# Optimization experiments

Measured on AMD Instinct MI355X. Metric: run time of the kernel, lower is better.

The kernel has to match this reference:

```python
import jax, jax.numpy as jnp
import numpy as np

B, LQ, LK, D, DV = 8, 2048, 2048, 128, 128


def setup_inputs() -> dict:
    key = jax.random.key(0)
    ks = jax.random.split(key, 6)
    return {
        "query": jax.random.normal(ks[0], (B, LQ, D), dtype=jnp.float32),
        "key": jax.random.normal(ks[1], (B, LK, D), dtype=jnp.float32),
        "value": jax.random.normal(ks[2], (B, LK, DV), dtype=jnp.float32),
        "Wq": jax.random.normal(ks[3], (D, D), dtype=jnp.float32) * 0.08,
        "Wk": jax.random.normal(ks[4], (D, D), dtype=jnp.float32) * 0.08,
        "Wv": jax.random.normal(ks[5], (DV, DV), dtype=jnp.float32) * 0.08,
        "attention_mask": jnp.ones((B, 1, LK), dtype=jnp.int32),
    }


def reference(query, key, value, Wq, Wk, Wv, attention_mask):
    # Linear projections (right-multiplication, as in `x @ W`)
    q = query @ Wq          # [B, lq, n_ed]
    k = key @ Wk            # [B, lk, n_ed]
    v = value @ Wv          # [B, lk, n_ev]
    scale = 1.0 / np.sqrt(q.shape[-1])
    scores = jnp.einsum("bqd,bkd->bqk", q, k) * scale  # [B, lq, lk]
    # additive mask: 0 where attend, -inf where mask==0 (broadcasts)
    mask_vals = jnp.where(attention_mask == 0, -jnp.inf, 0.0).astype(scores.dtype)
    scores = scores + mask_vals
    attn = jax.nn.softmax(scores, axis=-1)
    return attn @ v         # [B, lq, n_ev]
```

## Files before the change

### kernel.cpp

```cpp
#include <hip/hip_runtime.h>
#include <hip/hip_bf16.h>

typedef unsigned short u16;
typedef unsigned int u32;
typedef __attribute__((ext_vector_type(8))) short s8v;
typedef __attribute__((ext_vector_type(4))) float f4v;
typedef __attribute__((ext_vector_type(16))) float f16v;

#define B_N 8
#define L_Q 2048
#define L_K 2048
#define DIM 128
#define KT  64
#define KSPLIT 4
#define KCHUNK (L_K / KSPLIT)
#define NIT (KCHUNK / KT)

__device__ __forceinline__ u16 f2bf(float f) {
  union { float f; unsigned u; } v; v.f = f;
  return (u16)((v.u + 0x7fffu + ((v.u >> 16) & 1u)) >> 16);
}
__device__ __forceinline__ float bf2f(u16 u) {
  union { u32 u; float f; } v; v.u = ((u32)u) << 16; return v.f;
}
__device__ __forceinline__ u32 packbf2(float a, float b) {
  union { __hip_bfloat162 h; u32 u; } v;
  v.h = __float22bfloat162_rn(make_float2(a, b));
  return v.u;
}
__device__ __forceinline__ void async16(const u16* g, u16* l) {
  __builtin_amdgcn_global_load_lds(
      (const __attribute__((address_space(1))) u32*)(const void*)g,
      (__attribute__((address_space(3))) u32*)(void*)l, 16, 0, 0);
}


__global__ __launch_bounds__(256) void wprep(
    const float* __restrict__ Wq, const float* __restrict__ Wk,
    const float* __restrict__ Wv, u16* __restrict__ wbuf) {
  const int which = blockIdx.x;
  const int tid = threadIdx.x;
  const float* W = (which == 0) ? Wq : (which == 1) ? Wk : Wv;
  const float wscale = (which == 0) ? (1.44269504089f / 11.3137084990f) : 1.0f;
  u16* dst = wbuf + which * 16384;
#pragma unroll
  for (int i = 0; i < 16; ++i) {
    int f4i = tid + i * 256;
    float4 w4 = *(const float4*)(W + f4i * 4);
    int k = f4i >> 5, col = (f4i & 31) * 4;
    int ks = k >> 5, qd = (k & 31) >> 3, j = k & 7;
    float wv4[4] = {w4.x, w4.y, w4.z, w4.w};
#pragma unroll
    for (int c = 0; c < 4; ++c) {
      int n = col + c;
      dst[(ks * 8 + (n >> 4)) * 512 + (qd * 16 + (n & 15)) * 8 + j] = f2bf(wv4[c] * wscale);
    }
  }
}

__global__ __launch_bounds__(256, 3) void proj_mfma(
    const float* __restrict__ query, const float* __restrict__ key,
    const float* __restrict__ value, const u16* __restrict__ wbuf,
    u16* __restrict__ qp, u16* __restrict__ kp, u16* __restrict__ vp) {
  __shared__ __align__(16) u16 Wf[16384];
  __shared__ __align__(16) u16 Fb[8192];
  const int tid = threadIdx.x;
  const int bi = blockIdx.x;
  const int which = bi >> 8;
  const int sub = bi & 255;
  const int b = sub >> 5;
  const int rt = sub & 31;
  const float* X = (which == 0) ? query : (which == 1) ? key : value;
  const u16* Wfg = wbuf + which * 16384;

  const int w = tid >> 6, lane = tid & 63;
  const int ln = lane & 15, quad = lane >> 4;

#pragma unroll
  for (int c = 0; c < 8; ++c) {
    int cg = w * 8 + c;
    async16(Wfg + (size_t)(cg * 64 + lane) * 8, Wf + cg * 512);
  }

  const int xrow = rt * 64 + w * 16 + ln;
  const float* Xr = X + ((size_t)b * L_Q + xrow) * DIM;

  s8v a[4];
#pragma unroll
  for (int ks = 0; ks < 4; ++ks) {
    float4 xa = *(const float4*)(Xr + ks * 32 + quad * 8);
    float4 xb = *(const float4*)(Xr + ks * 32 + quad * 8 + 4);
    union { u32 wd[4]; s8v v; } t;
    t.wd[0] = packbf2(xa.x, xa.y);
    t.wd[1] = packbf2(xa.z, xa.w);
    t.wd[2] = packbf2(xb.x, xb.y);
    t.wd[3] = packbf2(xb.z, xb.w);
    a[ks] = t.v;
  }
  __syncthreads();

  f4v acc[8];
#pragma unroll
  for (int i = 0; i < 8; ++i) acc[i] = (f4v){0.f, 0.f, 0.f, 0.f};
#pragma unroll
  for (int ks = 0; ks < 4; ++ks)
#pragma unroll
    for (int nt = 0; nt < 8; ++nt) {
      s8v bw = *(const s8v*)(Wf + (ks * 8 + nt) * 512 + lane * 8);
      acc[nt] = __builtin_amdgcn_mfma_f32_16x16x32_bf16(a[ks], bw, acc[nt], 0, 0, 0);
    }

  if (which < 2) {
#pragma unroll
    for (int nt = 0; nt < 8; ++nt) {
      int base = ((w >> 1) * 8 + nt) * 512 + ((ln >> 3) * 32 + (w & 1) * 16 + quad * 4) * 8 + (ln & 7);
#pragma unroll
      for (int r = 0; r < 4; ++r) Fb[base + r * 8] = f2bf(acc[nt][r]);
    }
  } else {
#pragma unroll
    for (int nt = 0; nt < 8; ++nt) {
      int base = (w * 4 + (nt >> 1)) * 512 + ((quad >> 1) * 32 + (nt & 1) * 16 + ln) * 8 + (quad & 1) * 4;
      *(u32*)&Fb[base]     = packbf2(acc[nt][0], acc[nt][1]);
      *(u32*)&Fb[base + 2] = packbf2(acc[nt][2], acc[nt][3]);
    }
  }
  __syncthreads();

  u16* Y = ((which == 0) ? qp : (which == 1) ? kp : vp) + (size_t)(b * 32 + rt) * 8192;
#pragma unroll
  for (int r = 0; r < 4; ++r) {
    int c = tid + r * 256;
    *(s8v*)(Y + c * 8) = *(const s8v*)(Fb + c * 8);
  }
}

__global__ __launch_bounds__(256, 2) void flash_split(
    const u16* __restrict__ qp, const u16* __restrict__ kp,
    const u16* __restrict__ vp, const int* __restrict__ mask,
    u16* __restrict__ po, float* __restrict__ lbuf) {
  __shared__ __align__(16) u16 Kf[2][8192];
  __shared__ __align__(16) u16 Vf[2][8192];
  __shared__ float biasl[2][KT];

  const int tid = threadIdx.x;
  const int bi = blockIdx.x;
  const int b = bi & 7;
  const int rest = bi >> 3;
  const int p = rest & 3;
  const int qb = rest >> 2;
  const int w4 = tid >> 6;
  const int lane = tid & 63;
  const int qcol = lane & 31;
  const int H = lane >> 5;
  const bool Hb = (H != 0);

  const int* mb = mask + b * L_K;
  const int kt0 = p * NIT;

  auto stage = [&](int bufi, int kt_) {
    const u16* Ktile = kp + (size_t)(b * 32 + kt_) * 8192;
    const u16* Vtile = vp + (size_t)(b * 32 + kt_) * 8192;
#pragma unroll
    for (int c = 0; c < 4; ++c) {
      int f = w4 * 4 + c;
      async16(Ktile + (size_t)(f * 64 + lane) * 8, &Kf[bufi][f * 512]);
      async16(Vtile + (size_t)(f * 64 + lane) * 8, &Vf[bufi][f * 512]);
    }
  };

  const u16* Qt = qp + (size_t)(b * 64 + qb * 4 + w4) * 4096;
  s8v aq[8];
#pragma unroll
  for (int c = 0; c < 8; ++c) aq[c] = *(const s8v*)(Qt + c * 512 + lane * 8);

  f16v o[4];
#pragma unroll
  for (int i = 0; i < 4; ++i)
#pragma unroll
    for (int r = 0; r < 16; ++r) o[i][r] = 0.f;
  float lrow = 0.f;

  stage(0, kt0);
  int mv0 = mb[kt0 * KT + lane];
  bool ao_next = (__ballot(mv0 != 0) == ~0ull);
  if (!ao_next && tid < KT) biasl[0][tid] = (mv0 == 0) ? -__builtin_inff() : 0.f;
  __syncthreads();

  for (int it = 0; it < NIT; ++it) {
    const int cur = it & 1;
    const bool allones = ao_next;

    if (it + 1 < NIT) {
      stage(cur ^ 1, kt0 + it + 1);
      int mv = mb[(kt0 + it + 1) * KT + lane];
      ao_next = (__ballot(mv != 0) == ~0ull);
      if (!ao_next && tid < KT) biasl[cur ^ 1][tid] = (mv == 0) ? -__builtin_inff() : 0.f;
    }

    f16v s[2];
#pragma unroll
    for (int t = 0; t < 2; ++t)
#pragma unroll
      for (int r = 0; r < 16; ++r) s[t][r] = 0.f;
#pragma unroll
    for (int c = 0; c < 8; ++c) {
      s8v k0f = *(const s8v*)(&Kf[cur][c * 512] + lane * 8);
      s[0] = __builtin_amdgcn_mfma_f32_32x32x16_bf16(k0f, aq[c], s[0], 0, 0, 0);
      s8v k1f = *(const s8v*)(&Kf[cur][(8 + c) * 512] + lane * 8);
      s[1] = __builtin_amdgcn_mfma_f32_32x32x16_bf16(k1f, aq[c], s[1], 0, 0, 0);
    }
    if (!allones) {
#pragma unroll
      for (int t = 0; t < 2; ++t)
#pragma unroll
        for (int g = 0; g < 4; ++g) {
          float4 bt = *(const float4*)&biasl[cur][t * 32 + g * 8 + 4 * H];
          s[t][g * 4 + 0] += bt.x; s[t][g * 4 + 1] += bt.y;
          s[t][g * 4 + 2] += bt.z; s[t][g * 4 + 3] += bt.w;
        }
    }

    float rs = 0.f;
#pragma unroll
    for (int t = 0; t < 2; ++t)
#pragma unroll
      for (int r = 0; r < 16; ++r) {
        s[t][r] = __builtin_amdgcn_exp2f(s[t][r]);
        rs += s[t][r];
      }
    rs += __shfl_xor(rs, 32, 64);
    lrow += rs;

    u32 plo[2][4], phi[2][4];
#pragma unroll
    for (int t = 0; t < 2; ++t)
#pragma unroll
      for (int g = 0; g < 4; ++g) {
        plo[t][g] = packbf2(s[t][g * 4 + 0], s[t][g * 4 + 1]);
        phi[t][g] = packbf2(s[t][g * 4 + 2], s[t][g * 4 + 3]);
      }

#pragma unroll
    for (int kc = 0; kc < 4; ++kc) {
      const int t = kc >> 1, gl = (kc & 1) * 2;
      u32 a_lo0 = plo[t][gl], a_hi0 = phi[t][gl];
      u32 a_lo1 = plo[t][gl + 1], a_hi1 = phi[t][gl + 1];
      u32 snd_lo = Hb ? a_lo0 : a_lo1;
      u32 snd_hi = Hb ? a_hi0 : a_hi1;
      u32 r_lo = (u32)__shfl_xor((int)snd_lo, 32, 64);
      u32 r_hi = (u32)__shfl_xor((int)snd_hi, 32, 64);
      union { u32 wd[4]; s8v v; } pa;
      pa.wd[0] = Hb ? r_lo : a_lo0;
      pa.wd[1] = Hb ? r_hi : a_hi0;
      pa.wd[2] = Hb ? a_lo1 : r_lo;
      pa.wd[3] = Hb ? a_hi1 : r_hi;
#pragma unroll
      for (int ntv = 0; ntv < 4; ++ntv) {
        s8v bv = *(const s8v*)(&Vf[cur][(kc * 4 + ntv) * 512] + lane * 8);
        o[ntv] = __builtin_amdgcn_mfma_f32_32x32x16_bf16(pa.v, bv, o[ntv], 0, 0, 0);
      }
    }
    __syncthreads();
  }

#pragma unroll
  for (int ntv = 0; ntv < 4; ++ntv)
#pragma unroll
    for (int reg = 0; reg < 16; ++reg) {
      int qloc = (reg & 3) + 8 * (reg >> 2) + 4 * H;
      size_t q = (size_t)b * L_Q + qb * 128 + w4 * 32 + qloc;
      po[(q * KSPLIT + p) * DIM + ntv * 32 + qcol] = f2bf(o[ntv][reg]);
    }
  if (H == 0) {
    size_t q = (size_t)b * L_Q + qb * 128 + w4 * 32 + qcol;
    lbuf[q * KSPLIT + p] = lrow;
  }
}

__global__ __launch_bounds__(256) void combine(
    const u16* __restrict__ po, const float* __restrict__ lbuf,
    float* __restrict__ out) {
  const int t = threadIdx.x;
  const int lr = t >> 5, l32 = t & 31;
  const size_t q = (size_t)blockIdx.x * 8 + lr;

  float L = 0.f;
#pragma unroll
  for (int p = 0; p < KSPLIT; ++p) L += lbuf[q * KSPLIT + p];
  float invL = 1.0f / L;

  float4 acc = make_float4(0.f, 0.f, 0.f, 0.f);
#pragma unroll
  for (int p = 0; p < KSPLIT; ++p) {
    ushort4 u = *(const ushort4*)(po + (q * KSPLIT + p) * DIM + l32 * 4);
    acc.x += bf2f(u.x); acc.y += bf2f(u.y);
    acc.z += bf2f(u.z); acc.w += bf2f(u.w);
  }
  acc.x *= invL; acc.y *= invL; acc.z *= invL; acc.w *= invL;
  *(float4*)(out + q * DIM + l32 * 4) = acc;
}

extern "C" void kernel_launch(void* const* d_in, const int* in_sizes, int n_in,
                              void* d_out, int out_size, void* d_ws, size_t ws_size,
                              hipStream_t stream) {
  const float* query = (const float*)d_in[0];
  const float* key   = (const float*)d_in[1];
  const float* value = (const float*)d_in[2];
  const float* Wq    = (const float*)d_in[3];
  const float* Wk    = (const float*)d_in[4];
  const float* Wv    = (const float*)d_in[5];
  const int*   mask  = (const int*)d_in[6];
  float* out = (float*)d_out;

  u16* qp = (u16*)d_ws;
  u16* kp = qp + (size_t)B_N * L_Q * DIM;
  u16* vp = kp + (size_t)B_N * L_K * DIM;
  u16* po = vp + (size_t)B_N * DIM * L_K;
  float* lbuf = (float*)(po + (size_t)B_N * L_Q * KSPLIT * DIM);
  u16* wbuf = (u16*)(lbuf + (size_t)B_N * L_Q * KSPLIT);

  hipLaunchKernelGGL(wprep, dim3(3), dim3(256), 0, stream, Wq, Wk, Wv, wbuf);
  hipLaunchKernelGGL(proj_mfma, dim3(768), dim3(256), 0, stream,
                     query, key, value, wbuf, qp, kp, vp);
  hipLaunchKernelGGL(flash_split, dim3(512), dim3(256), 0, stream,
                     qp, kp, vp, mask, po, lbuf);
  hipLaunchKernelGGL(combine, dim3((B_N * L_Q) / 8), dim3(256), 0, stream,
                     po, lbuf, out);
}
```

Before: 117.9 us.

## Store split-K partial outputs in MFMA register layout with vectorized writes

The flash kernel now writes its partial outputs and row sums in the native MFMA accumulator fragment order, so each lane emits two 16-byte packed bf16 stores instead of 64 scattered 2-byte stores. The combine kernel is rewritten to read that fragment layout with vector loads, sum across splits, and scatter results to the row-major output using per-row inverse sums kept in shared memory. This targets the uncoalesced epilogue stores in the flash kernel. In exchange, the combine stage now does strided scalar fp32 output writes.

```diff
diff --git a/kernel.cpp b/kernel.cpp
--- a/kernel.cpp
+++ b/kernel.cpp
@@ -264,41 +264,62 @@
     __syncthreads();
   }
 
-#pragma unroll
-  for (int ntv = 0; ntv < 4; ++ntv)
-#pragma unroll
-    for (int reg = 0; reg < 16; ++reg) {
-      int qloc = (reg & 3) + 8 * (reg >> 2) + 4 * H;
-      size_t q = (size_t)b * L_Q + qb * 128 + w4 * 32 + qloc;
-      po[(q * KSPLIT + p) * DIM + ntv * 32 + qcol] = f2bf(o[ntv][reg]);
-    }
-  if (H == 0) {
-    size_t q = (size_t)b * L_Q + qb * 128 + w4 * 32 + qcol;
-    lbuf[q * KSPLIT + p] = lrow;
-  }
+  const size_t gidx = ((size_t)((p * 8 + b) * 16 + qb) * 4 + w4);
+  u16* pw = po + gidx * 4096 + (size_t)lane * 16;
+#pragma unroll
+  for (int ntv = 0; ntv < 4; ++ntv) {
+    union { u32 wd[4]; s8v v; } h1, h2;
+#pragma unroll
+    for (int j = 0; j < 4; ++j) {
+      h1.wd[j] = packbf2(o[ntv][2 * j], o[ntv][2 * j + 1]);
+      h2.wd[j] = packbf2(o[ntv][8 + 2 * j], o[ntv][9 + 2 * j]);
+    }
+    *(s8v*)(pw + ntv * 1024) = h1.v;
+    *(s8v*)(pw + ntv * 1024 + 8) = h2.v;
+  }
+  if (H == 0) lbuf[gidx * 32 + qcol] = lrow;
 }
 
 __global__ __launch_bounds__(256) void combine(
     const u16* __restrict__ po, const float* __restrict__ lbuf,
     float* __restrict__ out) {
-  const int t = threadIdx.x;
-  const int lr = t >> 5, l32 = t & 31;
-  const size_t q = (size_t)blockIdx.x * 8 + lr;
-
-  float L = 0.f;
-#pragma unroll
-  for (int p = 0; p < KSPLIT; ++p) L += lbuf[q * KSPLIT + p];
-  float invL = 1.0f / L;
-
-  float4 acc = make_float4(0.f, 0.f, 0.f, 0.f);
+  __shared__ float shL[32];
+  const int tid = threadIdx.x;
+  const int bi = blockIdx.x;
+  const int b = bi >> 6, qb = (bi >> 2) & 15, w4 = bi & 3;
+  const int wv = tid >> 6;
+  const int lane = tid & 63;
+  const int qcol = lane & 31;
+  const int H = lane >> 5;
+
+  float acc[16];
+#pragma unroll
+  for (int r = 0; r < 16; ++r) acc[r] = 0.f;
 #pragma unroll
   for (int p = 0; p < KSPLIT; ++p) {
-    ushort4 u = *(const ushort4*)(po + (q * KSPLIT + p) * DIM + l32 * 4);
-    acc.x += bf2f(u.x); acc.y += bf2f(u.y);
-    acc.z += bf2f(u.z); acc.w += bf2f(u.w);
-  }
-  acc.x *= invL; acc.y *= invL; acc.z *= invL; acc.w *= invL;
-  *(float4*)(out + q * DIM + l32 * 4) = acc;
+    const u16* src = po + ((size_t)((p * 8 + b) * 16 + qb) * 4 + w4) * 4096 + (size_t)(wv * 64 + lane) * 16;
+    s8v v1 = *(const s8v*)src;
+    s8v v2 = *(const s8v*)(src + 8);
+#pragma unroll
+    for (int r = 0; r < 8; ++r) {
+      acc[r] += bf2f((u16)v1[r]);
+      acc[8 + r] += bf2f((u16)v2[r]);
+    }
+  }
+  if (tid < 32) {
+    float L = 0.f;
+#pragma unroll
+    for (int p = 0; p < KSPLIT; ++p)
+      L += lbuf[((size_t)((p * 8 + b) * 16 + qb) * 4 + w4) * 32 + tid];
+    shL[tid] = 1.0f / L;
+  }
+  __syncthreads();
+#pragma unroll
+  for (int reg = 0; reg < 16; ++reg) {
+    int qloc = (reg & 3) + 8 * (reg >> 2) + 4 * H;
+    size_t q = (size_t)b * L_Q + qb * 128 + w4 * 32 + qloc;
+    out[q * DIM + wv * 32 + qcol] = acc[reg] * shL[qloc];
+  }
 }
 
 extern "C" void kernel_launch(void* const* d_in, const int* in_sizes, int n_in,
@@ -325,6 +346,6 @@
                      query, key, value, wbuf, qp, kp, vp);
   hipLaunchKernelGGL(flash_split, dim3(512), dim3(256), 0, stream,
                      qp, kp, vp, mask, po, lbuf);
-  hipLaunchKernelGGL(combine, dim3((B_N * L_Q) / 8), dim3(256), 0, stream,
+  hipLaunchKernelGGL(combine, dim3(512), dim3(256), 0, stream,
                      po, lbuf, out);
 }
```

Measured after the change: 119.3 us. No clear change (+1.2%).
